# Kernel optimization log

Measured on AMD Instinct MI355X. Metric: run time of the kernel, lower is better.

Reference implementation:

```python
import jax, jax.numpy as jnp
import numpy as np

N, X_DIM, Y_DIM, HID = 1024, 256, 256, 256  # HID = hidden_size // 2


def setup_inputs() -> dict:
    key = jax.random.key(0)
    ks = jax.random.split(key, 11)
    s_in = 1.0 / np.sqrt(X_DIM)
    s_h = 1.0 / np.sqrt(HID)
    return {
        "x_samples": jax.random.normal(ks[0], (N, X_DIM), jnp.float32),
        "y_samples": jax.random.normal(ks[1], (N, Y_DIM), jnp.float32),
        "z_samples": jax.random.normal(ks[2], (N, Y_DIM), jnp.float32),
        "w1_mu": jax.random.uniform(ks[3], (HID, X_DIM), jnp.float32, -s_in, s_in),
        "b1_mu": jax.random.uniform(ks[4], (HID,), jnp.float32, -s_in, s_in),
        "w2_mu": jax.random.uniform(ks[5], (Y_DIM, HID), jnp.float32, -s_h, s_h),
        "b2_mu": jax.random.uniform(ks[6], (Y_DIM,), jnp.float32, -s_h, s_h),
        "w1_lv": jax.random.uniform(ks[7], (HID, X_DIM), jnp.float32, -s_in, s_in),
        "b1_lv": jax.random.uniform(ks[8], (HID,), jnp.float32, -s_in, s_in),
        "w2_lv": jax.random.uniform(ks[9], (Y_DIM, HID), jnp.float32, -s_h, s_h),
        "b2_lv": jax.random.uniform(ks[10], (Y_DIM,), jnp.float32, -s_h, s_h),
    }


def reference(x_samples, y_samples, z_samples,
              w1_mu, b1_mu, w2_mu, b2_mu,
              w1_lv, b1_lv, w2_lv, b2_lv):
    # MLP heads (torch Linear: x @ W.T + b)
    h_mu = jax.nn.relu(x_samples @ w1_mu.T + b1_mu)
    mu = h_mu @ w2_mu.T + b2_mu                       # [N, D]
    h_lv = jax.nn.relu(x_samples @ w1_lv.T + b1_lv)
    logvar = jnp.tanh(h_lv @ w2_lv.T + b2_lv)          # [N, D]

    inv2var = 1.0 / (2.0 * jnp.exp(logvar))           # [N, D]

    # positive: per-sample conditional log-density term
    positive = -((mu - y_samples) ** 2 + (mu - z_samples) ** 2) * inv2var  # [N, D]

    # negative: mean over all pairings (i: prediction, j: sample)
    # pairwise squared diffs materialize [N, N, D] like the original broadcast
    pred = mu[:, None, :]                              # [N, 1, D]
    sq = (y_samples[None, :, :] - pred) ** 2 + (z_samples[None, :, :] - pred) ** 2
    negative = -sq.mean(axis=1) * inv2var              # [N, D]

    return jax.nn.relu(positive.sum(axis=-1) - negative.sum(axis=-1)).mean()
```

## Files before the change

kernel.cpp:

```cpp
#include <hip/hip_runtime.h>
#include <math.h>

constexpr int LSB = 72;

typedef short bf16x8 __attribute__((ext_vector_type(8)));
typedef float f32x4  __attribute__((ext_vector_type(4)));

__device__ __forceinline__ unsigned short f2bf_rne(float f) {
    unsigned u = __float_as_uint(f);
    unsigned r = (u + 0x7fff + ((u >> 16) & 1)) >> 16;
    return (unsigned short)r;
}
__device__ __forceinline__ float bf2f(unsigned short h) {
    return __uint_as_float(((unsigned)h) << 16);
}
__device__ __forceinline__ void split4(float4 v, ushort4& hi, ushort4& lo) {
    hi.x = f2bf_rne(v.x); lo.x = f2bf_rne(v.x - bf2f(hi.x));
    hi.y = f2bf_rne(v.y); lo.y = f2bf_rne(v.y - bf2f(hi.y));
    hi.z = f2bf_rne(v.z); lo.z = f2bf_rne(v.z - bf2f(hi.z));
    hi.w = f2bf_rne(v.w); lo.w = f2bf_rne(v.w - bf2f(hi.w));
}


__global__ __launch_bounds__(256)
void k1_layer1(const float* __restrict__ x,
               const float* __restrict__ w1m, const float* __restrict__ w1l,
               const float* __restrict__ b1m, const float* __restrict__ b1l,
               const float* __restrict__ w2m, const float* __restrict__ w2l,
               unsigned short* __restrict__ hmH, unsigned short* __restrict__ hmL,
               unsigned short* __restrict__ hlH, unsigned short* __restrict__ hlL,
               unsigned short* __restrict__ w2mH, unsigned short* __restrict__ w2mL,
               unsigned short* __restrict__ w2lH, unsigned short* __restrict__ w2lL,
               const float* __restrict__ y, const float* __restrict__ z,
               float* __restrict__ pA1, float* __restrict__ pB1,
               float* __restrict__ out) {
    const int bid = blockIdx.x, t = threadIdx.x;
    const int head = bid & 1, ct = (bid >> 1) & 7, rt = bid >> 4;
    const int rowBase = rt * 64, colBase = ct * 32;
    const int w = t >> 6, lane = t & 63, quad = lane >> 4, mr = lane & 15;

    const float* Bw   = head ? w1l : w1m;
    const float* bias = head ? b1l : b1m;
    unsigned short* CH = head ? hlH : hmH;
    unsigned short* CL = head ? hlL : hmL;

    __shared__ __align__(16) unsigned short Ah[64][LSB], Al[64][LSB];
    __shared__ __align__(16) unsigned short Bh[32][LSB], Bl[32][LSB];

    f32x4 acc[2] = {{0.f, 0.f, 0.f, 0.f}, {0.f, 0.f, 0.f, 0.f}};

    for (int kt = 0; kt < 256; kt += 64) {
#pragma unroll
        for (int p = 0; p < 4; p++) {
            int idx = p * 256 + t;
            int r = idx >> 4, k4 = idx & 15;
            float4 av = *(const float4*)&x[(rowBase + r) * 256 + kt + k4 * 4];
            ushort4 h4, l4;
            split4(av, h4, l4);
            *(ushort4*)&Ah[r][k4 * 4] = h4;
            *(ushort4*)&Al[r][k4 * 4] = l4;
            if (p < 2) {
                float4 bv = *(const float4*)&Bw[(colBase + r) * 256 + kt + k4 * 4];
                split4(bv, h4, l4);
                *(ushort4*)&Bh[r][k4 * 4] = h4;
                *(ushort4*)&Bl[r][k4 * 4] = l4;
            }
        }
        __syncthreads();

#pragma unroll
        for (int kk = 0; kk < 64; kk += 32) {
            int ko = kk + quad * 8;
            bf16x8 ah = *(const bf16x8*)&Ah[w * 16 + mr][ko];
            bf16x8 al = *(const bf16x8*)&Al[w * 16 + mr][ko];
#pragma unroll
            for (int nt = 0; nt < 2; nt++) {
                bf16x8 bh = *(const bf16x8*)&Bh[nt * 16 + mr][ko];
                bf16x8 bl = *(const bf16x8*)&Bl[nt * 16 + mr][ko];
                acc[nt] = __builtin_amdgcn_mfma_f32_16x16x32_bf16(ah, bh, acc[nt], 0, 0, 0);
                acc[nt] = __builtin_amdgcn_mfma_f32_16x16x32_bf16(ah, bl, acc[nt], 0, 0, 0);
                acc[nt] = __builtin_amdgcn_mfma_f32_16x16x32_bf16(al, bh, acc[nt], 0, 0, 0);
            }
        }
        __syncthreads();
    }

#pragma unroll
    for (int nt = 0; nt < 2; nt++) {
        int cg = colBase + nt * 16 + mr;
        float bb = bias[cg];
#pragma unroll
        for (int reg = 0; reg < 4; reg++) {
            int rg = rowBase + w * 16 + quad * 4 + reg;
            float v = fmaxf(acc[nt][reg] + bb, 0.f);
            unsigned short hi = f2bf_rne(v);
            CH[rg * 256 + cg] = hi;
            CL[rg * 256 + cg] = f2bf_rne(v - bf2f(hi));
        }
    }

    {
        int off = bid * 256 + t;
        float vm = w2m[off], vl = w2l[off];
        unsigned short h1 = f2bf_rne(vm);
        w2mH[off] = h1; w2mL[off] = f2bf_rne(vm - bf2f(h1));
        unsigned short h2 = f2bf_rne(vl);
        w2lH[off] = h2; w2lL[off] = f2bf_rne(vl - bf2f(h2));
    }

    {
        float sA = 0.f, sB = 0.f;
        int base = bid * 4 * 256 + t;
#pragma unroll
        for (int j = 0; j < 4; j++) {
            float yv = y[base + j * 256];
            float zv = z[base + j * 256];
            sA += yv * yv + zv * zv;
            sB += yv + zv;
        }
        pA1[bid * 256 + t] = sA;
        pB1[bid * 256 + t] = sB;
    }
    if (bid == 0 && t == 0) out[0] = 0.f;
}

__global__ __launch_bounds__(256)
void k2_layer2(const unsigned short* __restrict__ hmH, const unsigned short* __restrict__ hmL,
               const unsigned short* __restrict__ hlH, const unsigned short* __restrict__ hlL,
               const unsigned short* __restrict__ w2mH, const unsigned short* __restrict__ w2mL,
               const unsigned short* __restrict__ w2lH, const unsigned short* __restrict__ w2lL,
               const float* __restrict__ b2m, const float* __restrict__ b2l,
               float* __restrict__ muO, float* __restrict__ lvO,
               const float* __restrict__ pA1, const float* __restrict__ pB1,
               float* __restrict__ pA2, float* __restrict__ pB2) {
    const int bid = blockIdx.x, t = threadIdx.x;
    const int head = bid & 1, ct = (bid >> 1) & 7, rt = bid >> 4;
    const int rowBase = rt * 64, colBase = ct * 32;
    const int w = t >> 6, lane = t & 63, quad = lane >> 4, mr = lane & 15;

    const unsigned short* AH = head ? hlH : hmH;
    const unsigned short* AL = head ? hlL : hmL;
    const unsigned short* BH = head ? w2lH : w2mH;
    const unsigned short* BL = head ? w2lL : w2mL;
    const float* bias = head ? b2l : b2m;
    float* C = head ? lvO : muO;

    __shared__ __align__(16) unsigned short Ah[64][LSB], Al[64][LSB];
    __shared__ __align__(16) unsigned short Bh[32][LSB], Bl[32][LSB];

    f32x4 acc[2] = {{0.f, 0.f, 0.f, 0.f}, {0.f, 0.f, 0.f, 0.f}};

    for (int kt = 0; kt < 256; kt += 64) {
#pragma unroll
        for (int p = 0; p < 4; p++) {
            int idx = p * 256 + t;
            int r = idx >> 4, k4 = idx & 15;
            int off = (rowBase + r) * 256 + kt + k4 * 4;
            *(ushort4*)&Ah[r][k4 * 4] = *(const ushort4*)&AH[off];
            *(ushort4*)&Al[r][k4 * 4] = *(const ushort4*)&AL[off];
            if (p < 2) {
                int boff = (colBase + r) * 256 + kt + k4 * 4;
                *(ushort4*)&Bh[r][k4 * 4] = *(const ushort4*)&BH[boff];
                *(ushort4*)&Bl[r][k4 * 4] = *(const ushort4*)&BL[boff];
            }
        }
        __syncthreads();

#pragma unroll
        for (int kk = 0; kk < 64; kk += 32) {
            int ko = kk + quad * 8;
            bf16x8 ah = *(const bf16x8*)&Ah[w * 16 + mr][ko];
            bf16x8 al = *(const bf16x8*)&Al[w * 16 + mr][ko];
#pragma unroll
            for (int nt = 0; nt < 2; nt++) {
                bf16x8 bh = *(const bf16x8*)&Bh[nt * 16 + mr][ko];
                bf16x8 bl = *(const bf16x8*)&Bl[nt * 16 + mr][ko];
                acc[nt] = __builtin_amdgcn_mfma_f32_16x16x32_bf16(ah, bh, acc[nt], 0, 0, 0);
                acc[nt] = __builtin_amdgcn_mfma_f32_16x16x32_bf16(ah, bl, acc[nt], 0, 0, 0);
                acc[nt] = __builtin_amdgcn_mfma_f32_16x16x32_bf16(al, bh, acc[nt], 0, 0, 0);
            }
        }
        __syncthreads();
    }

#pragma unroll
    for (int nt = 0; nt < 2; nt++) {
        int cg = colBase + nt * 16 + mr;
        float bb = bias[cg];
#pragma unroll
        for (int reg = 0; reg < 4; reg++) {
            int rg = rowBase + w * 16 + quad * 4 + reg;
            C[rg * 256 + cg] = acc[nt][reg] + bb;
        }
    }

    if (bid < 16) {
        float sA = 0.f, sB = 0.f;
#pragma unroll
        for (int s = 0; s < 16; s++) {
            int o = (bid * 16 + s) * 256 + t;
            sA += pA1[o];
            sB += pB1[o];
        }
        pA2[bid * 256 + t] = sA;
        pB2[bid * 256 + t] = sB;
    }
}

__global__ __launch_bounds__(256)
void k3_epilogue(const float* __restrict__ muO, const float* __restrict__ lvO,
                 const float* __restrict__ y, const float* __restrict__ z,
                 const float* __restrict__ pA2, const float* __restrict__ pB2,
                 float* __restrict__ out) {
    __shared__ float red[4];
    int t = threadIdx.x;
    int lane = t & 63, wave = t >> 6;

    float mA = 0.f, mB = 0.f;
#pragma unroll
    for (int g = 0; g < 16; g++) {
        mA += pA2[g * 256 + t];
        mB += pB2[g * 256 + t];
    }
    mA *= (1.f / 1024.f);
    mB *= (1.f / 1024.f);

    float blockSum = 0.f;
    for (int r = 0; r < 4; r++) {
        int o = (blockIdx.x * 4 + r) * 256 + t;
        float m  = muO[o];
        float lv = tanhf(lvO[o]);
        float iv = 0.5f * expf(-lv);
        float yv = y[o];
        float zv = z[o];
        float Mt = mA - 2.f * m * mB + 2.f * m * m;
        float dy = m - yv, dz = m - zv;
        float term = iv * (Mt - dy * dy - dz * dz);
#pragma unroll
        for (int mask = 32; mask; mask >>= 1)
            term += __shfl_xor(term, mask, 64);
        if (lane == 0) red[wave] = term;
        __syncthreads();
        if (t == 0) {
            float rs = red[0] + red[1] + red[2] + red[3];
            blockSum += fmaxf(rs, 0.f);
        }
        __syncthreads();
    }
    if (t == 0) atomicAdd(out, blockSum * (1.f / 1024.f));
}

extern "C" void kernel_launch(void* const* d_in, const int* in_sizes, int n_in,
                              void* d_out, int out_size, void* d_ws, size_t ws_size,
                              hipStream_t stream) {
    const float* x   = (const float*)d_in[0];
    const float* y   = (const float*)d_in[1];
    const float* zs  = (const float*)d_in[2];
    const float* w1m = (const float*)d_in[3];
    const float* b1m = (const float*)d_in[4];
    const float* w2m = (const float*)d_in[5];
    const float* b2m = (const float*)d_in[6];
    const float* w1l = (const float*)d_in[7];
    const float* b1l = (const float*)d_in[8];
    const float* w2l = (const float*)d_in[9];
    const float* b2l = (const float*)d_in[10];
    float* out = (float*)d_out;

    char* ws = (char*)d_ws;
    float* pA1 = (float*)(ws);
    float* pB1 = (float*)(ws + (256u << 10));
    float* pA2 = (float*)(ws + (512u << 10));
    float* pB2 = (float*)(ws + (528u << 10));
    unsigned short* hmH = (unsigned short*)(ws + (1024u << 10));
    unsigned short* hmL = (unsigned short*)(ws + (1536u << 10));
    unsigned short* hlH = (unsigned short*)(ws + (2048u << 10));
    unsigned short* hlL = (unsigned short*)(ws + (2560u << 10));
    unsigned short* w2mH = (unsigned short*)(ws + (3072u << 10));
    unsigned short* w2mL = (unsigned short*)(ws + (3200u << 10));
    unsigned short* w2lH = (unsigned short*)(ws + (3328u << 10));
    unsigned short* w2lL = (unsigned short*)(ws + (3456u << 10));
    float* muO = (float*)(ws + (4096u << 10));
    float* lvO = (float*)(ws + (5120u << 10));

    k1_layer1<<<256, 256, 0, stream>>>(x, w1m, w1l, b1m, b1l, w2m, w2l,
                                       hmH, hmL, hlH, hlL,
                                       w2mH, w2mL, w2lH, w2lL,
                                       y, zs, pA1, pB1, out);
    k2_layer2<<<256, 256, 0, stream>>>(hmH, hmL, hlH, hlL,
                                       w2mH, w2mL, w2lH, w2lL,
                                       b2m, b2l, muO, lvO,
                                       pA1, pB1, pA2, pB2);
    k3_epilogue<<<256, 256, 0, stream>>>(muO, lvO, y, zs, pA2, pB2, out);
}
```

Measured before the change: 100.5 us.

## Fuse epilogue into layer-2 kernel using atomic tickets for last-block reductions

Measured after the change: 156.0 us. +55.2%, slower.

```diff
diff --git a/kernel.cpp b/kernel.cpp
--- a/kernel.cpp
+++ b/kernel.cpp
@@ -33,7 +33,8 @@
                unsigned short* __restrict__ w2lH, unsigned short* __restrict__ w2lL,
                const float* __restrict__ y, const float* __restrict__ z,
                float* __restrict__ pA1, float* __restrict__ pB1,
-               float* __restrict__ out) {
+               float* __restrict__ rowAcc, int* __restrict__ pairTick,
+               int* __restrict__ rowTick, float* __restrict__ out) {
     const int bid = blockIdx.x, t = threadIdx.x;
     const int head = bid & 1, ct = (bid >> 1) & 7, rt = bid >> 4;
     const int rowBase = rt * 64, colBase = ct * 32;
@@ -121,18 +122,26 @@
         pA1[bid * 256 + t] = sA;
         pB1[bid * 256 + t] = sB;
     }
+
+    if (bid < 4) rowAcc[bid * 256 + t] = 0.f;
+    if (bid == 4) {
+        if (t < 128) pairTick[t] = 0;
+        else if (t < 144) rowTick[t - 128] = 0;
+    }
     if (bid == 0 && t == 0) out[0] = 0.f;
 }
 
 __global__ __launch_bounds__(256)
-void k2_layer2(const unsigned short* __restrict__ hmH, const unsigned short* __restrict__ hmL,
-               const unsigned short* __restrict__ hlH, const unsigned short* __restrict__ hlL,
-               const unsigned short* __restrict__ w2mH, const unsigned short* __restrict__ w2mL,
-               const unsigned short* __restrict__ w2lH, const unsigned short* __restrict__ w2lL,
-               const float* __restrict__ b2m, const float* __restrict__ b2l,
-               float* __restrict__ muO, float* __restrict__ lvO,
-               const float* __restrict__ pA1, const float* __restrict__ pB1,
-               float* __restrict__ pA2, float* __restrict__ pB2) {
+void k2_fused(const unsigned short* __restrict__ hmH, const unsigned short* __restrict__ hmL,
+              const unsigned short* __restrict__ hlH, const unsigned short* __restrict__ hlL,
+              const unsigned short* __restrict__ w2mH, const unsigned short* __restrict__ w2mL,
+              const unsigned short* __restrict__ w2lH, const unsigned short* __restrict__ w2lL,
+              const float* __restrict__ b2m, const float* __restrict__ b2l,
+              float* __restrict__ muO, float* __restrict__ lvO,
+              const float* __restrict__ y, const float* __restrict__ z,
+              const float* __restrict__ pA1, const float* __restrict__ pB1,
+              float* __restrict__ rowAcc, int* __restrict__ pairTick,
+              int* __restrict__ rowTick, float* __restrict__ out) {
     const int bid = blockIdx.x, t = threadIdx.x;
     const int head = bid & 1, ct = (bid >> 1) & 7, rt = bid >> 4;
     const int rowBase = rt * 64, colBase = ct * 32;
@@ -147,6 +156,9 @@
 
     __shared__ __align__(16) unsigned short Ah[64][LSB], Al[64][LSB];
     __shared__ __align__(16) unsigned short Bh[32][LSB], Bl[32][LSB];
+    __shared__ float part[16][32];
+    __shared__ float mAf[32], mBf[32];
+    __shared__ int oldTick, oldRt;
 
     f32x4 acc[2] = {{0.f, 0.f, 0.f, 0.f}, {0.f, 0.f, 0.f, 0.f}};
 
@@ -194,60 +206,73 @@
         }
     }
 
-    if (bid < 16) {
+    __threadfence();
+    __syncthreads();
+    if (t == 0) oldTick = atomicAdd(&pairTick[bid >> 1], 1);
+    __syncthreads();
+    if (oldTick == 0) return;
+    __threadfence();
+
+    {
+        int c = t & 31, g = t >> 5;
+        int gc = ct * 32 + c;
         float sA = 0.f, sB = 0.f;
-#pragma unroll
-        for (int s = 0; s < 16; s++) {
-            int o = (bid * 16 + s) * 256 + t;
-            sA += pA1[o];
-            sB += pB1[o];
-        }
-        pA2[bid * 256 + t] = sA;
-        pB2[bid * 256 + t] = sB;
-    }
-}
-
-__global__ __launch_bounds__(256)
-void k3_epilogue(const float* __restrict__ muO, const float* __restrict__ lvO,
-                 const float* __restrict__ y, const float* __restrict__ z,
-                 const float* __restrict__ pA2, const float* __restrict__ pB2,
-                 float* __restrict__ out) {
-    __shared__ float red[4];
-    int t = threadIdx.x;
-    int lane = t & 63, wave = t >> 6;
-
-    float mA = 0.f, mB = 0.f;
-#pragma unroll
-    for (int g = 0; g < 16; g++) {
-        mA += pA2[g * 256 + t];
-        mB += pB2[g * 256 + t];
-    }
-    mA *= (1.f / 1024.f);
-    mB *= (1.f / 1024.f);
-
-    float blockSum = 0.f;
-    for (int r = 0; r < 4; r++) {
-        int o = (blockIdx.x * 4 + r) * 256 + t;
-        float m  = muO[o];
-        float lv = tanhf(lvO[o]);
-        float iv = 0.5f * expf(-lv);
-        float yv = y[o];
-        float zv = z[o];
-        float Mt = mA - 2.f * m * mB + 2.f * m * m;
-        float dy = m - yv, dz = m - zv;
-        float term = iv * (Mt - dy * dy - dz * dz);
-#pragma unroll
-        for (int mask = 32; mask; mask >>= 1)
-            term += __shfl_xor(term, mask, 64);
-        if (lane == 0) red[wave] = term;
-        __syncthreads();
-        if (t == 0) {
-            float rs = red[0] + red[1] + red[2] + red[3];
-            blockSum += fmaxf(rs, 0.f);
-        }
-        __syncthreads();
-    }
-    if (t == 0) atomicAdd(out, blockSum * (1.f / 1024.f));
+        for (int j = 0; j < 32; j++) {
+            int s = g * 32 + j;
+            sA += pA1[s * 256 + gc];
+            sB += pB1[s * 256 + gc];
+        }
+        part[g][c] = sA;
+        part[8 + g][c] = sB;
+    }
+    __syncthreads();
+    if (t < 32) {
+        float sA = 0.f, sB = 0.f;
+#pragma unroll
+        for (int g = 0; g < 8; g++) { sA += part[g][t]; sB += part[8 + g][t]; }
+        mAf[t] = sA * (1.f / 1024.f);
+        mBf[t] = sB * (1.f / 1024.f);
+    }
+    __syncthreads();
+
+    {
+        int col = t & 31, gcol = colBase + col;
+        float mA = mAf[col], mB = mBf[col];
+#pragma unroll
+        for (int r8 = 0; r8 < 8; r8++) {
+            int grow = rowBase + (t >> 5) * 8 + r8;
+            int o = grow * 256 + gcol;
+            float m  = muO[o];
+            float lv = tanhf(lvO[o]);
+            float iv = 0.5f * expf(-lv);
+            float yv = y[o];
+            float zv = z[o];
+            float Mt = mA - 2.f * m * mB + 2.f * m * m;
+            float dy = m - yv, dz = m - zv;
+            float term = iv * (Mt - dy * dy - dz * dz);
+#pragma unroll
+            for (int msk = 16; msk; msk >>= 1)
+                term += __shfl_xor(term, msk, 32);
+            if (col == 0) atomicAdd(&rowAcc[grow], term);
+        }
+    }
+
+    __threadfence();
+    __syncthreads();
+    if (t == 0) oldRt = atomicAdd(&rowTick[rt], 1);
+    __syncthreads();
+    if (oldRt != 7) return;
+    __threadfence();
+
+    if (t < 64) {
+        float v = fmaxf(__hip_atomic_load(&rowAcc[rt * 64 + t],
+                                          __ATOMIC_RELAXED,
+                                          __HIP_MEMORY_SCOPE_AGENT), 0.f);
+#pragma unroll
+        for (int msk = 32; msk; msk >>= 1)
+            v += __shfl_xor(v, msk, 64);
+        if (t == 0) atomicAdd(out, v * (1.f / 1024.f));
+    }
 }
 
 extern "C" void kernel_launch(void* const* d_in, const int* in_sizes, int n_in,
@@ -267,10 +292,11 @@
     float* out = (float*)d_out;
 
     char* ws = (char*)d_ws;
-    float* pA1 = (float*)(ws);
-    float* pB1 = (float*)(ws + (256u << 10));
-    float* pA2 = (float*)(ws + (512u << 10));
-    float* pB2 = (float*)(ws + (528u << 10));
+    float* pA1     = (float*)(ws);
+    float* pB1     = (float*)(ws + (256u << 10));
+    float* rowAcc  = (float*)(ws + (512u << 10));
+    int*   pairTick= (int*)(ws + (516u << 10));
+    int*   rowTick = (int*)(ws + (517u << 10));
     unsigned short* hmH = (unsigned short*)(ws + (1024u << 10));
     unsigned short* hmL = (unsigned short*)(ws + (1536u << 10));
     unsigned short* hlH = (unsigned short*)(ws + (2048u << 10));
@@ -285,10 +311,11 @@
     k1_layer1<<<256, 256, 0, stream>>>(x, w1m, w1l, b1m, b1l, w2m, w2l,
                                        hmH, hmL, hlH, hlL,
                                        w2mH, w2mL, w2lH, w2lL,
-                                       y, zs, pA1, pB1, out);
-    k2_layer2<<<256, 256, 0, stream>>>(hmH, hmL, hlH, hlL,
-                                       w2mH, w2mL, w2lH, w2lL,
-                                       b2m, b2l, muO, lvO,
-                                       pA1, pB1, pA2, pB2);
-    k3_epilogue<<<256, 256, 0, stream>>>(muO, lvO, y, zs, pA2, pB2, out);
-}
+                                       y, zs, pA1, pB1,
+                                       rowAcc, pairTick, rowTick, out);
+    k2_fused<<<256, 256, 0, stream>>>(hmH, hmL, hlH, hlL,
+                                      w2mH, w2mL, w2lH, w2lL,
+                                      b2m, b2l, muO, lvO,
+                                      y, zs, pA1, pB1,
+                                      rowAcc, pairTick, rowTick, out);
+}
```
